# Performance work log

Measured on AMD Instinct MI355X. Metric: run time of the kernel, lower is better.

Reference implementation:

```python
import jax, jax.numpy as jnp
import numpy as np

HIDDEN = 1024
B, S = 4, 2048


def setup_inputs() -> dict:
    key = jax.random.key(0)
    ks = jax.random.split(key, 8)
    scale = 1.0 / np.sqrt(HIDDEN)
    return {
        "hidden_states": jax.random.normal(ks[0], (B, S, HIDDEN), dtype=jnp.float32),
        "attention_mask": jnp.zeros((B, S, S), dtype=jnp.float32),
        "Wq": jax.random.normal(ks[1], (HIDDEN, HIDDEN), dtype=jnp.float32) * scale,
        "bq": jnp.zeros((HIDDEN,), dtype=jnp.float32),
        "Wk": jax.random.normal(ks[2], (HIDDEN, HIDDEN), dtype=jnp.float32) * scale,
        "bk": jnp.zeros((HIDDEN,), dtype=jnp.float32),
        "Wv": jax.random.normal(ks[3], (HIDDEN, HIDDEN), dtype=jnp.float32) * scale,
        "bv": jnp.zeros((HIDDEN,), dtype=jnp.float32),
    }


def reference(hidden_states, attention_mask, Wq, bq, Wk, bk, Wv, bv):
    # Dense projections (note: no head split in the original module)
    q = jnp.einsum('bsd,de->bse', hidden_states, Wq) + bq  # [B,S,H]
    k = jnp.einsum('bsd,de->bse', hidden_states, Wk) + bk
    v = jnp.einsum('bsd,de->bse', hidden_states, Wv) + bv
    # scores scaled by sqrt(hidden_size) (not per-head dim), per the source
    inv_scale = 1.0 / jnp.sqrt(jnp.asarray(q.shape[-1], dtype=q.dtype))
    scores = jnp.einsum('bqd,bkd->bqk', q, k) * inv_scale  # [B,S,S]
    scores = scores + attention_mask
    weights = jax.nn.softmax(scores, axis=-1)
    # dropout is identity (training=False)
    out = jnp.einsum('bqk,bkd->bqd', weights, v)  # [B,S,H]
    return out
```

## Files before the change

kernel.cpp:

```cpp
#include <hip/hip_runtime.h>
#include <stdint.h>

typedef __attribute__((ext_vector_type(8))) short short8;
typedef __attribute__((ext_vector_type(8))) unsigned short u16x8;
typedef __attribute__((ext_vector_type(4))) float f32x4;

__device__ __forceinline__ uint16_t f2bf(float x) {
  uint32_t u = __float_as_uint(x);
  uint32_t r = (u + 0x7FFFu + ((u >> 16) & 1u)) >> 16;
  return (uint16_t)r;
}
__device__ __forceinline__ float bf2f(uint16_t x) {
  return __uint_as_float(((uint32_t)x) << 16);
}

__device__ __forceinline__ void gl_lds16(const uint16_t* g, void* l) {
  __builtin_amdgcn_global_load_lds(
      (const __attribute__((address_space(1))) void*)g,
      (__attribute__((address_space(3))) void*)l, 16, 0, 0);
}


__global__ __launch_bounds__(256) void cvt_f32_to_bf16(const float* __restrict__ in,
                                                       uint16_t* __restrict__ out) {
  long i = ((long)blockIdx.x * 256 + threadIdx.x) * 8;
  f32x4 v0 = *(const f32x4*)(in + i);
  f32x4 v1 = *(const f32x4*)(in + i + 4);
  u16x8 o;
  o[0] = f2bf(v0[0]); o[1] = f2bf(v0[1]); o[2] = f2bf(v0[2]); o[3] = f2bf(v0[3]);
  o[4] = f2bf(v1[0]); o[5] = f2bf(v1[1]); o[6] = f2bf(v1[2]); o[7] = f2bf(v1[3]);
  *(u16x8*)(out + i) = o;
}

__global__ __launch_bounds__(64) void cvt_w_transpose(const float* __restrict__ W0,
                                                      const float* __restrict__ W1,
                                                      const float* __restrict__ W2,
                                                      uint16_t* __restrict__ WT) {
  const int z = blockIdx.z;
  const float* W = (z == 0) ? W0 : ((z == 1) ? W1 : W2);
  uint16_t* out = WT + (long)z * 1024 * 1024;
  const int n = blockIdx.x * 64 + threadIdx.x;
  const int k0 = blockIdx.y * 128;
  for (int kk = 0; kk < 128; kk += 8) {
    u16x8 o;
#pragma unroll
    for (int j = 0; j < 8; j++) o[j] = f2bf(W[(long)(k0 + kk + j) * 1024 + n]);
    *(u16x8*)(out + (long)n * 1024 + k0 + kk) = o;
  }
}

__global__ __launch_bounds__(256) void transpose_v(const uint16_t* __restrict__ V,
                                                   uint16_t* __restrict__ Vt) {
  __shared__ uint16_t tile[64][66];
  const int b = blockIdx.z;
  const int s0 = blockIdx.x * 64, d0 = blockIdx.y * 64;
  const int t = threadIdx.x;
  const int r = t >> 3, c = (t & 7) * 8;
  const uint16_t* Vb = V + (long)b * 2048 * 1024;
#pragma unroll
  for (int j = 0; j < 2; j++) {
    u16x8 v = *(const u16x8*)(Vb + (long)(s0 + r + 32 * j) * 1024 + d0 + c);
#pragma unroll
    for (int i = 0; i < 8; i++) tile[r + 32 * j][c + i] = v[i];
  }
  __syncthreads();
  uint16_t* Vtb = Vt + (long)b * 1024 * 2048;
#pragma unroll
  for (int j = 0; j < 2; j++) {
    const int d = r + 32 * j;
    u16x8 o;
#pragma unroll
    for (int i = 0; i < 8; i++) o[i] = tile[c + i][d];
    *(u16x8*)(Vtb + (long)(d0 + d) * 2048 + s0 + c) = o;
  }
}

template <int MODE>
__global__ __launch_bounds__(256) void gemm_bt(
    const uint16_t* __restrict__ Abase, long sAz,
    const uint16_t* __restrict__ Bbase, long sBz,
    int K, int N,
    char* __restrict__ Cbase, long sCz,
    const float* __restrict__ e0, const float* __restrict__ e1,
    const float* __restrict__ e2,
    const float* __restrict__ lsum) {
  __shared__ uint16_t Al[2][128 * 32];
  __shared__ uint16_t Bl[2][128 * 32];
  const int t = threadIdx.x;
  const int lane = t & 63;
  const int w = t >> 6;
  const int bm = blockIdx.x, bn = blockIdx.y, bz = blockIdx.z;

  const uint16_t* A = (const uint16_t*)((const char*)Abase + (long)bz * sAz);
  const uint16_t* Bm = (const uint16_t*)((const char*)Bbase + (long)bz * sBz);

  const int sr = t >> 2;
  const int sc = (t & 3) * 8;
  const uint16_t* ga0 = A + (long)(bm * 128 + sr) * K + sc;
  const uint16_t* ga1 = A + (long)(bm * 128 + 64 + sr) * K + sc;
  const uint16_t* gb0 = Bm + (long)(bn * 128 + sr) * K + sc;
  const uint16_t* gb1 = Bm + (long)(bn * 128 + 64 + sr) * K + sc;

  f32x4 acc[4][4];
#pragma unroll
  for (int i = 0; i < 4; i++)
#pragma unroll
    for (int j = 0; j < 4; j++) acc[i][j] = (f32x4){0.f, 0.f, 0.f, 0.f};

  const int wm = w >> 1, wn = w & 1;
  const int fr = lane & 15, kg = lane >> 4;
  const int aoff = (wm * 64 + fr) * 32 + kg * 8;
  const int boff = (wn * 64 + fr) * 32 + kg * 8;

  gl_lds16(ga0, Al[0] + w * 512);
  gl_lds16(ga1, Al[0] + 2048 + w * 512);
  gl_lds16(gb0, Bl[0] + w * 512);
  gl_lds16(gb1, Bl[0] + 2048 + w * 512);

  int cur = 0;
  for (int k0 = 0; k0 < K; k0 += 32) {
    __syncthreads();
    if (k0 + 32 < K) {
      const int nb = cur ^ 1, kn = k0 + 32;
      gl_lds16(ga0 + kn, Al[nb] + w * 512);
      gl_lds16(ga1 + kn, Al[nb] + 2048 + w * 512);
      gl_lds16(gb0 + kn, Bl[nb] + w * 512);
      gl_lds16(gb1 + kn, Bl[nb] + 2048 + w * 512);
    }
    const uint16_t* Ab = Al[cur];
    const uint16_t* Bb = Bl[cur];
    short8 a[4], b[4];
#pragma unroll
    for (int i = 0; i < 4; i++) a[i] = *(const short8*)(Ab + aoff + i * 16 * 32);
#pragma unroll
    for (int j = 0; j < 4; j++) b[j] = *(const short8*)(Bb + boff + j * 16 * 32);
#pragma unroll
    for (int i = 0; i < 4; i++)
#pragma unroll
      for (int j = 0; j < 4; j++)
        acc[i][j] = __builtin_amdgcn_mfma_f32_16x16x32_bf16(a[i], b[j], acc[i][j], 0, 0, 0);
    cur ^= 1;
  }

  const int row0 = bm * 128 + wm * 64 + (kg << 2);
  const int col0 = bn * 128 + wn * 64 + fr;

  if (MODE == 0) {
    const float* bias = (bz == 0) ? e0 : ((bz == 1) ? e1 : e2);
    uint16_t* C = (uint16_t*)(Cbase + (long)bz * sCz);
#pragma unroll
    for (int i = 0; i < 4; i++) {
#pragma unroll
      for (int j = 0; j < 4; j++) {
        const float bv_ = bias[col0 + j * 16];
#pragma unroll
        for (int r = 0; r < 4; r++) {
          C[(long)(row0 + i * 16 + r) * N + col0 + j * 16] = f2bf(acc[i][j][r] + bv_);
        }
      }
    }
  } else {
    float* C = (float*)(Cbase + (long)bz * sCz);
    const float* ls = lsum + (long)bz * 2048;
#pragma unroll
    for (int i = 0; i < 4; i++) {
      const float ri0 = 1.0f / ls[row0 + i * 16];
      const float ri1 = 1.0f / ls[row0 + i * 16 + 1];
      const float ri2 = 1.0f / ls[row0 + i * 16 + 2];
      const float ri3 = 1.0f / ls[row0 + i * 16 + 3];
#pragma unroll
      for (int j = 0; j < 4; j++) {
        float* dst = C + (long)(row0 + i * 16) * N + col0 + j * 16;
        dst[0] = acc[i][j][0] * ri0;
        dst[(long)N] = acc[i][j][1] * ri1;
        dst[(long)2 * N] = acc[i][j][2] * ri2;
        dst[(long)3 * N] = acc[i][j][3] * ri3;
      }
    }
  }
}

__global__ __launch_bounds__(512, 2) void gemm_sc(
    const uint16_t* __restrict__ Abase, long sAz,
    const uint16_t* __restrict__ Bbase, long sBz,
    int K, int N,
    char* __restrict__ Cbase, long sCz,
    const float* __restrict__ maskb, long sMz, float scale,
    float* __restrict__ lsum) {
  constexpr int ABYTES = 32768;
  constexpr int BUFB = 65536;
  __shared__ __align__(16) char lds[2 * BUFB];
  const int t = threadIdx.x;
  const int lane = t & 63;
  const int w = t >> 6;
  const int bm = blockIdx.x, bn = blockIdx.y, bz = blockIdx.z;
  const uint16_t* A = (const uint16_t*)((const char*)Abase + (long)bz * sAz);
  const uint16_t* B = (const uint16_t*)((const char*)Bbase + (long)bz * sBz);

  const int srow = t >> 3;
  const int scol = ((((t & 7) * 16) ^ ((srow & 7) << 4)) >> 1);
  const uint16_t* gA[4];
  const uint16_t* gB[4];
#pragma unroll
  for (int s = 0; s < 4; s++) {
    gA[s] = A + (long)(bm * 256 + s * 64 + srow) * K + scol;
    gB[s] = B + (long)(bn * 256 + s * 64 + srow) * K + scol;
  }

  const int wm = w >> 2, wn = w & 3;
  const int fr = lane & 15, kg = lane >> 4;
  const int X = (fr & 7) << 4;
  const int aRow = (wm * 128 + fr) * 128 + kg * 16;
  const int bRow = (wn * 64 + fr) * 128 + kg * 16;

  f32x4 acc[8][4];
#pragma unroll
  for (int i = 0; i < 8; i++)
#pragma unroll
    for (int j = 0; j < 4; j++) acc[i][j] = (f32x4){0.f, 0.f, 0.f, 0.f};

  short8 aR[4][2], bR[4][2];
  const int NT = K >> 6;

#define ARD(off, i, ks) (*(const short8*)(lds + (off) + ((aRow + (i) * 2048 + (ks) * 64) ^ X)))
#define BRD(off, j, ks) (*(const short8*)(lds + ABYTES + (off) + ((bRow + (j) * 2048 + (ks) * 64) ^ X)))
#define STG_A01(off, ko) { gl_lds16(gA[0] + (ko), lds + (off) + w * 1024); \
                           gl_lds16(gA[1] + (ko), lds + (off) + 8192 + w * 1024); }
#define STG_A23(off, ko) { gl_lds16(gA[2] + (ko), lds + (off) + 16384 + w * 1024); \
                           gl_lds16(gA[3] + (ko), lds + (off) + 24576 + w * 1024); }
#define STG_B01(off, ko) { gl_lds16(gB[0] + (ko), lds + ABYTES + (off) + w * 1024); \
                           gl_lds16(gB[1] + (ko), lds + ABYTES + (off) + 8192 + w * 1024); }
#define STG_B23(off, ko) { gl_lds16(gB[2] + (ko), lds + ABYTES + (off) + 16384 + w * 1024); \
                           gl_lds16(gB[3] + (ko), lds + ABYTES + (off) + 24576 + w * 1024); }
#define LGKM0 { asm volatile("s_waitcnt lgkmcnt(0)" ::: "memory"); __builtin_amdgcn_sched_barrier(0); }
#define MFMA16(I0, J0)                                                            \
  __builtin_amdgcn_s_setprio(1);                                                  \
  _Pragma("unroll") for (int i = 0; i < 4; i++)                                   \
  _Pragma("unroll") for (int j = 0; j < 2; j++)                                   \
  _Pragma("unroll") for (int ks = 0; ks < 2; ks++)                                \
    acc[(I0) + i][(J0) + j] = __builtin_amdgcn_mfma_f32_16x16x32_bf16(            \
        aR[i][ks], bR[(J0) + j][ks], acc[(I0) + i][(J0) + j], 0, 0, 0);           \
  __builtin_amdgcn_s_setprio(0);

  STG_A01(0, 0); STG_A23(0, 0); STG_B01(0, 0); STG_B23(0, 0);

  int curo = 0;
  for (int tt = 0; tt < NT - 1; ++tt) {
    const int nxto = curo ^ BUFB;
    const int ko = (tt + 1) << 6;
    STG_A01(nxto, ko);
    asm volatile("s_waitcnt vmcnt(2)" ::: "memory");
    __builtin_amdgcn_s_barrier();
    __builtin_amdgcn_sched_barrier(0);
#pragma unroll
    for (int i = 0; i < 4; i++) { aR[i][0] = ARD(curo, i, 0); aR[i][1] = ARD(curo, i, 1); }
#pragma unroll
    for (int j = 0; j < 4; j++) { bR[j][0] = BRD(curo, j, 0); bR[j][1] = BRD(curo, j, 1); }
    LGKM0;
    MFMA16(0, 0);
    __builtin_amdgcn_s_barrier();
    STG_A23(nxto, ko);
    __builtin_amdgcn_s_barrier();
    MFMA16(0, 2);
    __builtin_amdgcn_s_barrier();
    STG_B01(nxto, ko);
#pragma unroll
    for (int i = 0; i < 4; i++) { aR[i][0] = ARD(curo, 4 + i, 0); aR[i][1] = ARD(curo, 4 + i, 1); }
    __builtin_amdgcn_s_barrier();
    LGKM0;
    MFMA16(4, 2);
    __builtin_amdgcn_s_barrier();
    STG_B23(nxto, ko);
    __builtin_amdgcn_s_barrier();
    MFMA16(4, 0);
    __builtin_amdgcn_s_barrier();
    curo = nxto;
  }
  asm volatile("s_waitcnt vmcnt(0)" ::: "memory");
  __builtin_amdgcn_s_barrier();
  __builtin_amdgcn_sched_barrier(0);
#pragma unroll
  for (int i = 0; i < 4; i++) { aR[i][0] = ARD(curo, i, 0); aR[i][1] = ARD(curo, i, 1); }
#pragma unroll
  for (int j = 0; j < 4; j++) { bR[j][0] = BRD(curo, j, 0); bR[j][1] = BRD(curo, j, 1); }
  LGKM0;
  MFMA16(0, 0);
  MFMA16(0, 2);
#pragma unroll
  for (int i = 0; i < 4; i++) { aR[i][0] = ARD(curo, 4 + i, 0); aR[i][1] = ARD(curo, 4 + i, 1); }
  LGKM0;
  MFMA16(4, 2);
  MFMA16(4, 0);

  __syncthreads();
  constexpr int RS = 260;
  float* eL = (float*)lds;
  const int wboff = wm * (16 * RS) + (kg * 4) * RS + wn * 64 + fr;
  const int lr = t >> 4, slab = lr >> 4, row16 = lr & 15, cj = t & 15;
  const float* rb = eL + slab * (16 * RS) + row16 * RS + cj * 16;
  const int grow_base = bm * 256 + slab * 128 + row16;
  const int colg = bn * 256 + cj * 16;
  uint16_t* Cw = (uint16_t*)(Cbase + (long)bz * sCz);
  const float* mk = (const float*)((const char*)maskb + (long)bz * sMz);

#pragma unroll
  for (int i = 0; i < 8; i++) {
#pragma unroll
    for (int j = 0; j < 4; j++)
#pragma unroll
      for (int r = 0; r < 4; r++)
        eL[wboff + r * RS + j * 16] = acc[i][j][r];
    __syncthreads();
    f32x4 v0 = *(const f32x4*)(rb);
    f32x4 v1 = *(const f32x4*)(rb + 4);
    f32x4 v2 = *(const f32x4*)(rb + 8);
    f32x4 v3 = *(const f32x4*)(rb + 12);
    const int grow = grow_base + i * 16;
    const float* mrow = mk + (long)grow * N + colg;
    f32x4 m0 = *(const f32x4*)(mrow);
    f32x4 m1 = *(const f32x4*)(mrow + 4);
    f32x4 m2 = *(const f32x4*)(mrow + 8);
    f32x4 m3 = *(const f32x4*)(mrow + 12);
    float e[16];
#pragma unroll
    for (int q = 0; q < 4; q++) {
      e[q] = __expf(v0[q] * scale + m0[q]);
      e[4 + q] = __expf(v1[q] * scale + m1[q]);
      e[8 + q] = __expf(v2[q] * scale + m2[q]);
      e[12 + q] = __expf(v3[q] * scale + m3[q]);
    }
    float ps = 0.f;
#pragma unroll
    for (int q = 0; q < 16; q++) ps += e[q];
    ps += __shfl_xor(ps, 1);
    ps += __shfl_xor(ps, 2);
    ps += __shfl_xor(ps, 4);
    ps += __shfl_xor(ps, 8);
    if ((lane & 15) == 0) atomicAdd(lsum + (long)bz * 2048 + grow, ps);
    u16x8 o0, o1;
#pragma unroll
    for (int q = 0; q < 8; q++) { o0[q] = f2bf(e[q]); o1[q] = f2bf(e[8 + q]); }
    uint16_t* dst = Cw + (long)grow * N + colg;
    *(u16x8*)dst = o0;
    *(u16x8*)(dst + 8) = o1;
    __syncthreads();
  }
#undef ARD
#undef BRD
#undef STG_A01
#undef STG_A23
#undef STG_B01
#undef STG_B23
#undef LGKM0
#undef MFMA16
}

extern "C" void kernel_launch(void* const* d_in, const int* in_sizes, int n_in,
                              void* d_out, int out_size, void* d_ws, size_t ws_size,
                              hipStream_t stream) {
  const float* hs = (const float*)d_in[0];
  const float* mask = (const float*)d_in[1];
  const float* Wq = (const float*)d_in[2];
  const float* bq = (const float*)d_in[3];
  const float* Wk = (const float*)d_in[4];
  const float* bk = (const float*)d_in[5];
  const float* Wv = (const float*)d_in[6];
  const float* bv = (const float*)d_in[7];
  float* out = (float*)d_out;

  char* ws = (char*)d_ws;
  uint16_t* hsb = (uint16_t*)ws;
  uint16_t* WT = (uint16_t*)(ws + (16L << 20));
  uint16_t* QKV = (uint16_t*)(ws + (22L << 20));
  uint16_t* Vt = (uint16_t*)(ws + (70L << 20));
  uint16_t* E = (uint16_t*)(ws + (86L << 20));
  float* lsum = (float*)(ws + (118L << 20));

  cvt_f32_to_bf16<<<4096, 256, 0, stream>>>(hs, hsb);
  cvt_w_transpose<<<dim3(16, 8, 3), 64, 0, stream>>>(Wq, Wk, Wv, WT);
  hipMemsetAsync((void*)lsum, 0, 4L * 2048 * sizeof(float), stream);
  gemm_bt<0><<<dim3(64, 8, 3), 256, 0, stream>>>(
      hsb, 0L, WT, 2L << 20, 1024, 1024, (char*)QKV, 16L << 20,
      bq, bk, bv, nullptr);
  transpose_v<<<dim3(32, 16, 4), 256, 0, stream>>>(QKV + 2L * 8192 * 1024, Vt);
  gemm_sc<<<dim3(8, 8, 4), 512, 0, stream>>>(
      QKV, 4L << 20, QKV + 8192L * 1024, 4L << 20, 1024, 2048, (char*)E, 8L << 20,
      mask, 16L << 20, 0.03125f, lsum);
  gemm_bt<2><<<dim3(16, 8, 4), 256, 0, stream>>>(
      E, 8L << 20, Vt, 4L << 20, 2048, 1024, (char*)out, 8L << 20,
      nullptr, nullptr, nullptr, lsum);
}
```

Before: 196.5 us.

## Enlarge GEMM tiles to 256x128 with 512 threads and fuse QKV projection

The generic GEMM kernel grows from a 128x128 tile with 256 threads to a 256x128 tile with 512 threads (8 waves, two blocks per CU). Each staged B tile is now reused across twice as many A rows. The QKV projection launches as a single N=3072 GEMM over the concatenated transposed weights, and the output slab and bias are chosen from the column block. The goal is less global/LDS traffic per FLOP and fewer, larger blocks. In exchange the grid has fewer blocks, which may hurt load balance on the PV GEMM (256 blocks), and LDS use per block grows.

```diff
diff --git a/kernel.cpp b/kernel.cpp
--- a/kernel.cpp
+++ b/kernel.cpp
@@ -76,7 +76,7 @@
 }
 
 template <int MODE>
-__global__ __launch_bounds__(256) void gemm_bt(
+__global__ __launch_bounds__(512, 2) void gemm3(
     const uint16_t* __restrict__ Abase, long sAz,
     const uint16_t* __restrict__ Bbase, long sBz,
     int K, int N,
@@ -84,22 +84,22 @@
     const float* __restrict__ e0, const float* __restrict__ e1,
     const float* __restrict__ e2,
     const float* __restrict__ lsum) {
-  __shared__ uint16_t Al[2][128 * 32];
-  __shared__ uint16_t Bl[2][128 * 32];
+  constexpr int ABYTES = 256 * 32 * 2;
+  constexpr int BBYTES = 128 * 32 * 2;
+  constexpr int BUFB = ABYTES + BBYTES;
+  __shared__ __align__(16) char lds[2 * BUFB];
   const int t = threadIdx.x;
   const int lane = t & 63;
   const int w = t >> 6;
   const int bm = blockIdx.x, bn = blockIdx.y, bz = blockIdx.z;
-
   const uint16_t* A = (const uint16_t*)((const char*)Abase + (long)bz * sAz);
   const uint16_t* Bm = (const uint16_t*)((const char*)Bbase + (long)bz * sBz);
 
   const int sr = t >> 2;
   const int sc = (t & 3) * 8;
-  const uint16_t* ga0 = A + (long)(bm * 128 + sr) * K + sc;
-  const uint16_t* ga1 = A + (long)(bm * 128 + 64 + sr) * K + sc;
+  const uint16_t* ga0 = A + (long)(bm * 256 + sr) * K + sc;
+  const uint16_t* ga1 = A + (long)(bm * 256 + 128 + sr) * K + sc;
   const uint16_t* gb0 = Bm + (long)(bn * 128 + sr) * K + sc;
-  const uint16_t* gb1 = Bm + (long)(bn * 128 + 64 + sr) * K + sc;
 
   f32x4 acc[4][4];
 #pragma unroll
@@ -112,23 +112,20 @@
   const int aoff = (wm * 64 + fr) * 32 + kg * 8;
   const int boff = (wn * 64 + fr) * 32 + kg * 8;
 
-  gl_lds16(ga0, Al[0] + w * 512);
-  gl_lds16(ga1, Al[0] + 2048 + w * 512);
-  gl_lds16(gb0, Bl[0] + w * 512);
-  gl_lds16(gb1, Bl[0] + 2048 + w * 512);
+#define STG(off, ko) { gl_lds16(ga0 + (ko), lds + (off) + w * 1024); \
+                       gl_lds16(ga1 + (ko), lds + (off) + 8192 + w * 1024); \
+                       gl_lds16(gb0 + (ko), lds + (off) + ABYTES + w * 1024); }
+
+  STG(0, 0);
 
   int cur = 0;
   for (int k0 = 0; k0 < K; k0 += 32) {
     __syncthreads();
     if (k0 + 32 < K) {
-      const int nb = cur ^ 1, kn = k0 + 32;
-      gl_lds16(ga0 + kn, Al[nb] + w * 512);
-      gl_lds16(ga1 + kn, Al[nb] + 2048 + w * 512);
-      gl_lds16(gb0 + kn, Bl[nb] + w * 512);
-      gl_lds16(gb1 + kn, Bl[nb] + 2048 + w * 512);
+      STG((cur ^ 1) * BUFB, k0 + 32);
     }
-    const uint16_t* Ab = Al[cur];
-    const uint16_t* Bb = Bl[cur];
+    const uint16_t* Ab = (const uint16_t*)(lds + cur * BUFB);
+    const uint16_t* Bb = (const uint16_t*)(lds + cur * BUFB + ABYTES);
     short8 a[4], b[4];
 #pragma unroll
     for (int i = 0; i < 4; i++) a[i] = *(const short8*)(Ab + aoff + i * 16 * 32);
@@ -141,36 +138,37 @@
         acc[i][j] = __builtin_amdgcn_mfma_f32_16x16x32_bf16(a[i], b[j], acc[i][j], 0, 0, 0);
     cur ^= 1;
   }
-
-  const int row0 = bm * 128 + wm * 64 + (kg << 2);
-  const int col0 = bn * 128 + wn * 64 + fr;
-
+#undef STG
+
+  const int row0 = bm * 256 + wm * 64 + (kg << 2);
   if (MODE == 0) {
-    const float* bias = (bz == 0) ? e0 : ((bz == 1) ? e1 : e2);
-    uint16_t* C = (uint16_t*)(Cbase + (long)bz * sCz);
+    const int zz = bn >> 3;
+    const float* bias = (zz == 0) ? e0 : ((zz == 1) ? e1 : e2);
+    uint16_t* C = (uint16_t*)(Cbase + (long)zz * sCz);
+    const int cb = (bn & 7) * 128 + wn * 64 + fr;
 #pragma unroll
     for (int i = 0; i < 4; i++) {
 #pragma unroll
       for (int j = 0; j < 4; j++) {
-        const float bv_ = bias[col0 + j * 16];
+        const float bv_ = bias[cb + j * 16];
 #pragma unroll
         for (int r = 0; r < 4; r++) {
-          C[(long)(row0 + i * 16 + r) * N + col0 + j * 16] = f2bf(acc[i][j][r] + bv_);
+          C[(long)(row0 + i * 16 + r) * 1024 + cb + j * 16] = f2bf(acc[i][j][r] + bv_);
         }
       }
     }
   } else {
+    const int col0 = bn * 128 + wn * 64 + fr;
     float* C = (float*)(Cbase + (long)bz * sCz);
     const float* ls = lsum + (long)bz * 2048;
 #pragma unroll
     for (int i = 0; i < 4; i++) {
-      const float ri0 = 1.0f / ls[row0 + i * 16];
-      const float ri1 = 1.0f / ls[row0 + i * 16 + 1];
-      const float ri2 = 1.0f / ls[row0 + i * 16 + 2];
-      const float ri3 = 1.0f / ls[row0 + i * 16 + 3];
+      const int rr = row0 + i * 16;
+      const float ri0 = 1.0f / ls[rr], ri1 = 1.0f / ls[rr + 1];
+      const float ri2 = 1.0f / ls[rr + 2], ri3 = 1.0f / ls[rr + 3];
 #pragma unroll
       for (int j = 0; j < 4; j++) {
-        float* dst = C + (long)(row0 + i * 16) * N + col0 + j * 16;
+        float* dst = C + (long)rr * N + col0 + j * 16;
         dst[0] = acc[i][j][0] * ri0;
         dst[(long)N] = acc[i][j][1] * ri1;
         dst[(long)2 * N] = acc[i][j][2] * ri2;
@@ -379,14 +377,14 @@
   cvt_f32_to_bf16<<<4096, 256, 0, stream>>>(hs, hsb);
   cvt_w_transpose<<<dim3(16, 8, 3), 64, 0, stream>>>(Wq, Wk, Wv, WT);
   hipMemsetAsync((void*)lsum, 0, 4L * 2048 * sizeof(float), stream);
-  gemm_bt<0><<<dim3(64, 8, 3), 256, 0, stream>>>(
-      hsb, 0L, WT, 2L << 20, 1024, 1024, (char*)QKV, 16L << 20,
+  gemm3<0><<<dim3(32, 24, 1), 512, 0, stream>>>(
+      hsb, 0L, WT, 0L, 1024, 3072, (char*)QKV, 16L << 20,
       bq, bk, bv, nullptr);
   transpose_v<<<dim3(32, 16, 4), 256, 0, stream>>>(QKV + 2L * 8192 * 1024, Vt);
   gemm_sc<<<dim3(8, 8, 4), 512, 0, stream>>>(
       QKV, 4L << 20, QKV + 8192L * 1024, 4L << 20, 1024, 2048, (char*)E, 8L << 20,
       mask, 16L << 20, 0.03125f, lsum);
-  gemm_bt<2><<<dim3(16, 8, 4), 256, 0, stream>>>(
+  gemm3<2><<<dim3(8, 8, 4), 512, 0, stream>>>(
       E, 8L << 20, Vt, 4L << 20, 2048, 1024, (char*)out, 8L << 20,
       nullptr, nullptr, nullptr, lsum);
 }
```

New measurement: 196.4 us. Within noise of the previous version (-0.1%).
